# Performance work log

Measured on AMD Instinct MI355X. Metric: run time of the kernel, lower is better.

Reference implementation:

```python
import jax, jax.numpy as jnp
import numpy as np

CS = 64          # chunk_size
CP = CS - 1      # causal_padding
H = 8            # heads
DH = 64          # dim_head
SCALE = DH ** -0.5


def rotate_half(x):
    x1, x2 = jnp.split(x, 2, axis=-1)
    return jnp.concatenate((-x2, x1), axis=-1)


def apply_rope(t, freqs):
    rd = freqs.shape[-1]
    t_rot, t_pass = t[..., :rd], t[..., rd:]
    t_rot = t_rot * jnp.cos(freqs) + rotate_half(t_rot) * jnp.sin(freqs)
    return jnp.concatenate((t_rot, t_pass), axis=-1)


def setup_inputs() -> dict:
    key = jax.random.key(0)
    ks = jax.random.split(key, 10)
    b, n, dim = 4, 4096, 1024
    k_chunks, r, rlen = 64, 2, 128
    inner = H * DH
    return {
        "x": jax.random.normal(ks[0], (b, n, dim), dtype=jnp.float32),
        "context": jax.random.normal(ks[1], (b, k_chunks, r, rlen, dim), dtype=jnp.float32),
        "q_pos_emb": jax.random.normal(ks[2], (1, 1, CS, DH), dtype=jnp.float32),
        "k_pos_emb": jax.random.normal(ks[3], (1, 1, rlen, DH), dtype=jnp.float32),
        "Wq": jax.random.normal(ks[4], (dim, inner), dtype=jnp.float32) * 0.02,
        "Wk": jax.random.normal(ks[5], (dim, inner), dtype=jnp.float32) * 0.02,
        "Wv": jax.random.normal(ks[6], (dim, inner), dtype=jnp.float32) * 0.02,
        "Wo": jax.random.normal(ks[7], (inner, dim), dtype=jnp.float32) * 0.02,
        "bo": jnp.zeros((dim,), dtype=jnp.float32),
        "null_k": jax.random.normal(ks[8], (inner,), dtype=jnp.float32),
        "null_v": jax.random.normal(ks[9], (inner,), dtype=jnp.float32),
    }


def reference(x, context, q_pos_emb, k_pos_emb, Wq, Wk, Wv, Wo, bo, null_k, null_v):
    b, n, dim = x.shape
    _, k_chunks, r, rlen, _ = context.shape
    # causal shift: drop first CP tokens, pad CP zeros at end (F.pad with -CP)
    xs = jnp.pad(x[:, CP:], ((0, 0), (0, CP), (0, 0)))
    seq_index = (n // CS) * CS
    rem = n - seq_index
    xs = xs[:, :seq_index]                                   # [b, k*CS, dim]
    # shift q rope the same way; pad region gets freqs=0 -> identity rotation
    qpe = jnp.pad(q_pos_emb[:, :, CP:], ((0, 0), (0, 0), (0, CP), (0, 0)))
    kpe = jnp.tile(k_pos_emb, (1, 1, r, 1))                  # [1,1,r*rlen,DH]
    bk = b * k_chunks
    xc = xs.reshape(bk, CS, dim)
    ctx = context.reshape(bk, r * rlen, dim)
    # projections -> [bk, h, seq, dh]
    q = (xc @ Wq).reshape(bk, CS, H, DH).transpose(0, 2, 1, 3) * SCALE
    k = (ctx @ Wk).reshape(bk, r * rlen, H, DH).transpose(0, 2, 1, 3)
    v = (ctx @ Wv).reshape(bk, r * rlen, H, DH).transpose(0, 2, 1, 3)
    q = apply_rope(q, qpe)
    k = apply_rope(k, kpe)
    # null kv prepend
    nk = jnp.broadcast_to(null_k.reshape(1, H, 1, DH), (bk, H, 1, DH))
    nv = jnp.broadcast_to(null_v.reshape(1, H, 1, DH), (bk, H, 1, DH))
    k = jnp.concatenate((nk, k), axis=2)
    v = jnp.concatenate((nv, v), axis=2)
    sim = jnp.einsum('bhid,bhjd->bhij', q, k)
    attn = jax.nn.softmax(sim, axis=-1)
    o = jnp.einsum('bhij,bhjd->bhid', attn, v)
    o = o.transpose(0, 2, 1, 3).reshape(bk, CS, H * DH)
    o = o @ Wo + bo                                          # [bk, CS, dim]
    o = o.reshape(b, k_chunks * CS, dim)
    # unshift: pad CP zeros at front, trim CP - rem from end
    o = jnp.concatenate(
        (jnp.zeros((b, CP, dim), o.dtype), o[:, :k_chunks * CS - CP + rem]), axis=1)
    return o
```

## Files before the change

kernel.cpp:

```cpp
#include <hip/hip_runtime.h>


#define DEV __device__ __forceinline__

typedef __bf16 bf16x8 __attribute__((ext_vector_type(8)));
typedef float f32x4 __attribute__((ext_vector_type(4)));

DEV unsigned short f2bf(float f) {
  union { float f; unsigned int u; } v; v.f = f;
  unsigned int u = v.u;
  unsigned int r = (u + 0x7FFFu + ((u >> 16) & 1u)) >> 16;
  return (unsigned short)r;
}
DEV float bf2f(unsigned short h) {
  union { unsigned int u; float f; } v; v.u = ((unsigned int)h) << 16;
  return v.f;
}

DEV void ldst16(const void* g, void* l) {
  __builtin_amdgcn_global_load_lds(
      (const __attribute__((address_space(1))) void*)g,
      (__attribute__((address_space(3))) void*)l, 16, 0, 0);
}

__global__ __launch_bounds__(256) void prep_k(const float* __restrict__ Wq,
                                              const float* __restrict__ Wk,
                                              const float* __restrict__ Wv,
                                              const float* __restrict__ Wo,
                                              const float* __restrict__ qpe,
                                              const float* __restrict__ kpe,
                                              unsigned short* __restrict__ Wqt,
                                              unsigned short* __restrict__ Wkt,
                                              unsigned short* __restrict__ Wvt,
                                              unsigned short* __restrict__ Wot,
                                              float* __restrict__ ck, float* __restrict__ sk,
                                              float* __restrict__ cq, float* __restrict__ sq,
                                              float* __restrict__ out) {
  int blk = blockIdx.x;
  if (blk < 8192) {
    int idx = blk * 256 + threadIdx.x;
    int which = idx >> 19;
    int loc = idx & 524287;
    if (which < 3) {
      int k = loc & 1023, n = loc >> 10;
      const float* W = which == 0 ? Wq : (which == 1 ? Wk : Wv);
      unsigned short* Wt = which == 0 ? Wqt : (which == 1 ? Wkt : Wvt);
      float scale = which == 0 ? 0.125f : 1.0f;
      Wt[loc] = f2bf(W[(size_t)k * 512 + n] * scale);
    } else {
      int k = loc & 511, n = loc >> 9;
      Wot[loc] = f2bf(Wo[(size_t)k * 1024 + n]);
    }
  } else if (blk < 8444) {
    int r = blk - 8192;
    int b = r / 63, rr = r % 63;
    float4 z = {0.f, 0.f, 0.f, 0.f};
    *(float4*)(out + (((size_t)(b * 4096 + rr)) << 10) + threadIdx.x * 4) = z;
  } else {
    int t = (blk - 8444) * 256 + threadIdx.x;
    float f = kpe[t];
    ck[t] = cosf(f);
    sk[t] = sinf(f);
    if (t < 64) {
      float g = qpe[63 * 64 + t];
      cq[t] = cosf(g);
      sq[t] = sinf(g);
    }
  }
}

__global__ __launch_bounds__(256) void cast_k(const float* __restrict__ ctx,
                                              const float* __restrict__ x,
                                              unsigned short* __restrict__ ctxb,
                                              unsigned short* __restrict__ xq) {
  int blk = blockIdx.x;
  if (blk < 32768) {
    size_t i = ((size_t)blk * 256 + threadIdx.x) * 8;
    float4 a = *(const float4*)(ctx + i);
    float4 b = *(const float4*)(ctx + i + 4);
    union { uint4 v; unsigned short s[8]; } u;
    u.s[0] = f2bf(a.x); u.s[1] = f2bf(a.y); u.s[2] = f2bf(a.z); u.s[3] = f2bf(a.w);
    u.s[4] = f2bf(b.x); u.s[5] = f2bf(b.y); u.s[6] = f2bf(b.z); u.s[7] = f2bf(b.w);
    *(uint4*)(ctxb + i) = u.v;
  } else {
    size_t flat = ((size_t)(blk - 32768) * 256 + threadIdx.x) * 8;
    int row = (int)(flat >> 10);
    int c = (int)(flat & 1023);
    int b = row >> 12, p = row & 4095;
    union { uint4 v; unsigned short s[8]; } u;
    if (p <= 4032) {
      const float* sp = x + (((size_t)(b << 12) + p + 63) << 10) + c;
      float4 a = *(const float4*)sp;
      float4 d = *(const float4*)(sp + 4);
      u.s[0] = f2bf(a.x); u.s[1] = f2bf(a.y); u.s[2] = f2bf(a.z); u.s[3] = f2bf(a.w);
      u.s[4] = f2bf(d.x); u.s[5] = f2bf(d.y); u.s[6] = f2bf(d.z); u.s[7] = f2bf(d.w);
    } else {
      #pragma unroll
      for (int e = 0; e < 8; ++e) u.s[e] = 0;
    }
    *(uint4*)(xq + flat) = u.v;
  }
}

template <int MODE>
__global__ __launch_bounds__(256) void gemm_proj(const unsigned short* __restrict__ A,
                                                 const unsigned short* __restrict__ B0,
                                                 const unsigned short* __restrict__ B1,
                                                 unsigned short* __restrict__ out0,
                                                 unsigned short* __restrict__ out1,
                                                 const float* __restrict__ ck,
                                                 const float* __restrict__ sk,
                                                 const float* __restrict__ cq,
                                                 const float* __restrict__ sq,
                                                 int M, int K) {
  __shared__ unsigned short sh[16384];
  unsigned short* As = sh;
  unsigned short* Bs = sh + 8192;

  int id = blockIdx.x;
  int x, y, z;
  if (MODE == 0) { y = id & 3; x = id >> 2; z = 0; }
  else           { y = id & 3; z = (id >> 2) & 1; x = id >> 3; }
  const unsigned short* B = z ? B1 : B0;
  int m0 = x * 128, n0 = y * 128;
  int tid = threadIdx.x, w = tid >> 6, lane = tid & 63;
  int wm = (w & 1) * 64, wn = (w >> 1) * 64;
  int Lrow = lane >> 3, Lc = lane & 7;
  int srcC = Lc ^ (Lrow & 7);

  f32x4 acc[4][4] = {};

  for (int k0 = 0; k0 < K; k0 += 64) {
    #pragma unroll
    for (int q = 0; q < 4; ++q) {
      int t = w * 4 + q;
      ldst16(A + (size_t)(m0 + t * 8 + Lrow) * K + (k0 + srcC * 8), (char*)As + t * 1024);
      ldst16(B + (size_t)(n0 + t * 8 + Lrow) * K + (k0 + srcC * 8), (char*)Bs + t * 1024);
    }
    __syncthreads();
    #pragma unroll
    for (int k32 = 0; k32 < 2; ++k32) {
      int c = k32 * 4 + (lane >> 4);
      bf16x8 af[4], bfr[4];
      #pragma unroll
      for (int mt = 0; mt < 4; ++mt) {
        int m = wm + mt * 16 + (lane & 15);
        af[mt] = *(const bf16x8*)((const char*)As + m * 128 + (c ^ (m & 7)) * 16);
      }
      #pragma unroll
      for (int nt = 0; nt < 4; ++nt) {
        int n = wn + nt * 16 + (lane & 15);
        bfr[nt] = *(const bf16x8*)((const char*)Bs + n * 128 + (c ^ (n & 7)) * 16);
      }
      #pragma unroll
      for (int mt = 0; mt < 4; ++mt)
        #pragma unroll
        for (int nt = 0; nt < 4; ++nt)
          acc[mt][nt] = __builtin_amdgcn_mfma_f32_16x16x32_bf16(af[mt], bfr[nt], acc[mt][nt], 0, 0, 0);
    }
    __syncthreads();
  }

  if (MODE == 0) {
    #pragma unroll
    for (int mt = 0; mt < 4; ++mt)
      #pragma unroll
      for (int nt = 0; nt < 4; ++nt)
        #pragma unroll
        for (int r = 0; r < 4; ++r) {
          int m = m0 + wm + mt * 16 + (lane >> 4) * 4 + r;
          int n = n0 + wn + nt * 16 + (lane & 15);
          float val = acc[mt][nt][r];
          if ((m & 63) == 0) {
            int d = nt * 16 + (lane & 15);
            float partner = acc[mt][nt ^ 2][r];
            val = val * cq[d] + (nt < 2 ? -partner : partner) * sq[d];
          }
          out0[(size_t)m * 512 + n] = f2bf(val);
        }
  } else if (z == 0) {
    #pragma unroll
    for (int mt = 0; mt < 4; ++mt)
      #pragma unroll
      for (int r = 0; r < 4; ++r) {
        int m = m0 + wm + mt * 16 + (lane >> 4) * 4 + r;
        int fib = (m & 127) * 64;
        #pragma unroll
        for (int nt = 0; nt < 4; ++nt) {
          int n = n0 + wn + nt * 16 + (lane & 15);
          int d = nt * 16 + (lane & 15);
          float partner = acc[mt][nt ^ 2][r];
          float val = acc[mt][nt][r] * ck[fib + d] + (nt < 2 ? -partner : partner) * sk[fib + d];
          out0[(size_t)m * 512 + n] = f2bf(val);
        }
      }
  } else {
    #pragma unroll
    for (int mt = 0; mt < 4; ++mt)
      #pragma unroll
      for (int nt = 0; nt < 4; ++nt)
        #pragma unroll
        for (int r = 0; r < 4; ++r) {
          int ml = wm + mt * 16 + (lane >> 4) * 4 + r;
          int nl = wn + nt * 16 + (lane & 15);
          int mc = ml >> 3, me = ml & 7;
          *(unsigned short*)((char*)sh + nl * 256 + ((mc ^ (nl & 15)) * 16) + me * 2) =
              f2bf(acc[mt][nt][r]);
        }
    __syncthreads();
    #pragma unroll
    for (int i = 0; i < 8; ++i) {
      int flat = i * 256 + tid;
      int nl = flat >> 4, mc = flat & 15;
      uint4 v = *(const uint4*)((const char*)sh + nl * 256 + ((mc ^ (nl & 15)) * 16));
      *(uint4*)(out1 + (size_t)(n0 + nl) * M + m0 + mc * 8) = v;
    }
  }
}

__global__ __launch_bounds__(256) void gemm_out(const unsigned short* __restrict__ A,
                                                const unsigned short* __restrict__ B,
                                                const float* __restrict__ bias,
                                                float* __restrict__ out) {
  __shared__ unsigned short sh[16384];
  unsigned short* As = sh;
  unsigned short* Bs = sh + 8192;
  const int K = 512, N = 1024;
  int id = blockIdx.x;
  int y = id & 7, x = id >> 3;
  int m0 = x * 128, n0 = y * 128;
  int tid = threadIdx.x, w = tid >> 6, lane = tid & 63;
  int wm = (w & 1) * 64, wn = (w >> 1) * 64;
  int Lrow = lane >> 3, Lc = lane & 7;
  int srcC = Lc ^ (Lrow & 7);

  f32x4 acc[4][4] = {};

  for (int k0 = 0; k0 < K; k0 += 64) {
    #pragma unroll
    for (int q = 0; q < 4; ++q) {
      int t = w * 4 + q;
      ldst16(A + (size_t)(m0 + t * 8 + Lrow) * K + (k0 + srcC * 8), (char*)As + t * 1024);
      ldst16(B + (size_t)(n0 + t * 8 + Lrow) * K + (k0 + srcC * 8), (char*)Bs + t * 1024);
    }
    __syncthreads();
    #pragma unroll
    for (int k32 = 0; k32 < 2; ++k32) {
      int c = k32 * 4 + (lane >> 4);
      bf16x8 af[4], bfr[4];
      #pragma unroll
      for (int mt = 0; mt < 4; ++mt) {
        int m = wm + mt * 16 + (lane & 15);
        af[mt] = *(const bf16x8*)((const char*)As + m * 128 + (c ^ (m & 7)) * 16);
      }
      #pragma unroll
      for (int nt = 0; nt < 4; ++nt) {
        int n = wn + nt * 16 + (lane & 15);
        bfr[nt] = *(const bf16x8*)((const char*)Bs + n * 128 + (c ^ (n & 7)) * 16);
      }
      #pragma unroll
      for (int mt = 0; mt < 4; ++mt)
        #pragma unroll
        for (int nt = 0; nt < 4; ++nt)
          acc[mt][nt] = __builtin_amdgcn_mfma_f32_16x16x32_bf16(af[mt], bfr[nt], acc[mt][nt], 0, 0, 0);
    }
    __syncthreads();
  }
  #pragma unroll
  for (int mt = 0; mt < 4; ++mt)
    #pragma unroll
    for (int nt = 0; nt < 4; ++nt)
      #pragma unroll
      for (int r = 0; r < 4; ++r) {
        int m = m0 + wm + mt * 16 + (lane >> 4) * 4 + r;
        int n = n0 + wn + nt * 16 + (lane & 15);
        int b = m >> 12, t = m & 4095;
        if (t <= 4032)
          out[((size_t)((b << 12) + t + 63)) * N + n] = acc[mt][nt][r] + bias[n];
      }
}

__global__ __launch_bounds__(256) void attn_kernel(const unsigned short* __restrict__ qb,
                                                   const unsigned short* __restrict__ kb,
                                                   const unsigned short* __restrict__ vtg,
                                                   const float* __restrict__ nullk,
                                                   const float* __restrict__ nullv,
                                                   unsigned short* __restrict__ ob) {
  __shared__ unsigned short qs[64 * 64];
  __shared__ unsigned short ks[256 * 64];
  __shared__ unsigned short ps[64 * 256];
  __shared__ float rnull[64];
  __shared__ float rsum[64];
  int id = blockIdx.x;
  int bc = (id & 7) + 8 * (id >> 6);
  int h = (id >> 3) & 7;
  int tid = threadIdx.x, w = tid >> 6, lane = tid & 63;
  int Lrow = lane >> 3, Lc = lane & 7, srcC = Lc ^ (Lrow & 7);

  #pragma unroll
  for (int q8 = 0; q8 < 2; ++q8) {
    int t = w * 2 + q8;
    ldst16(qb + (size_t)(bc * 64 + t * 8 + Lrow) * 512 + h * 64 + srcC * 8, (char*)qs + t * 1024);
  }
  #pragma unroll
  for (int q8 = 0; q8 < 8; ++q8) {
    int t = w * 8 + q8;
    ldst16(kb + (size_t)(bc * 256 + t * 8 + Lrow) * 512 + h * 64 + srcC * 8, (char*)ks + t * 1024);
  }
  __syncthreads();

  {
    int rl = lane >> 2, part = lane & 3;
    int row = w * 16 + rl;
    float s = 0.f;
    #pragma unroll
    for (int e = 0; e < 16; ++e) {
      int d = part * 16 + e;
      unsigned short qv = *(const unsigned short*)((const char*)qs + row * 128 +
                                                   (((d >> 3) ^ (row & 7)) * 16) + (d & 7) * 2);
      s += bf2f(qv) * nullk[h * 64 + d];
    }
    s += __shfl_xor(s, 1);
    s += __shfl_xor(s, 2);
    if (part == 0) rnull[row] = s;
  }

  f32x4 acc[16] = {};
  #pragma unroll
  for (int k32 = 0; k32 < 2; ++k32) {
    int c = k32 * 4 + (lane >> 4);
    int m = w * 16 + (lane & 15);
    bf16x8 a = *(const bf16x8*)((const char*)qs + m * 128 + (c ^ (m & 7)) * 16);
    #pragma unroll
    for (int nt = 0; nt < 16; ++nt) {
      int n = nt * 16 + (lane & 15);
      bf16x8 b = *(const bf16x8*)((const char*)ks + n * 128 + (c ^ (n & 7)) * 16);
      acc[nt] = __builtin_amdgcn_mfma_f32_16x16x32_bf16(a, b, acc[nt], 0, 0, 0);
    }
  }

  int g = lane >> 4;
  #pragma unroll
  for (int r = 0; r < 4; ++r) {
    int row = w * 16 + g * 4 + r;
    float mx = -3.0e38f;
    #pragma unroll
    for (int nt = 0; nt < 16; ++nt) mx = fmaxf(mx, acc[nt][r]);
    mx = fmaxf(mx, __shfl_xor(mx, 1));
    mx = fmaxf(mx, __shfl_xor(mx, 2));
    mx = fmaxf(mx, __shfl_xor(mx, 4));
    mx = fmaxf(mx, __shfl_xor(mx, 8));
    float ns = rnull[row];
    float mm = fmaxf(mx, ns);
    float s = 0.f;
    #pragma unroll
    for (int nt = 0; nt < 16; ++nt) {
      float p = __expf(acc[nt][r] - mm);
      acc[nt][r] = p;
      s += p;
    }
    s += __shfl_xor(s, 1);
    s += __shfl_xor(s, 2);
    s += __shfl_xor(s, 4);
    s += __shfl_xor(s, 8);
    float en = __expf(ns - mm);
    s += en;
    if ((lane & 15) == 0) {
      rsum[row] = s;
      rnull[row] = en;
    }
  }

  #pragma unroll
  for (int nt = 0; nt < 16; ++nt)
    #pragma unroll
    for (int r = 0; r < 4; ++r) {
      int row = w * 16 + g * 4 + r;
      int col = nt * 16 + (lane & 15);
      *(unsigned short*)((char*)ps + row * 512 + (((col >> 3) ^ (row & 7)) * 16) + (col & 7) * 2) =
          f2bf(acc[nt][r]);
    }
  __syncthreads();

  #pragma unroll
  for (int q8 = 0; q8 < 8; ++q8) {
    int t = w * 8 + q8;
    int dd = t * 2 + (lane >> 5);
    int cl = (lane & 31) ^ (dd & 7);
    ldst16(vtg + (size_t)(h * 64 + dd) * 65536 + bc * 256 + cl * 8, (char*)ks + t * 1024);
  }
  __syncthreads();

  f32x4 oacc[4] = {};
  #pragma unroll
  for (int k32 = 0; k32 < 8; ++k32) {
    int c = k32 * 4 + (lane >> 4);
    int m = w * 16 + (lane & 15);
    bf16x8 a = *(const bf16x8*)((const char*)ps + m * 512 + (c ^ (m & 7)) * 16);
    #pragma unroll
    for (int nt = 0; nt < 4; ++nt) {
      int n = nt * 16 + (lane & 15);
      bf16x8 b = *(const bf16x8*)((const char*)ks + n * 512 + (c ^ (n & 7)) * 16);
      oacc[nt] = __builtin_amdgcn_mfma_f32_16x16x32_bf16(a, b, oacc[nt], 0, 0, 0);
    }
  }
  #pragma unroll
  for (int nt = 0; nt < 4; ++nt)
    #pragma unroll
    for (int r = 0; r < 4; ++r) {
      int row = w * 16 + g * 4 + r;
      int d = nt * 16 + (lane & 15);
      float o = oacc[nt][r] + rnull[row] * nullv[h * 64 + d];
      o /= rsum[row];
      ob[((size_t)(bc * 64 + row) * 8 + h) * 64 + d] = f2bf(o);
    }
}

extern "C" void kernel_launch(void* const* d_in, const int* in_sizes, int n_in,
                              void* d_out, int out_size, void* d_ws, size_t ws_size,
                              hipStream_t stream) {
  const float* x = (const float*)d_in[0];
  const float* ctx = (const float*)d_in[1];
  const float* qpe = (const float*)d_in[2];
  const float* kpe = (const float*)d_in[3];
  const float* Wq = (const float*)d_in[4];
  const float* Wk = (const float*)d_in[5];
  const float* Wv = (const float*)d_in[6];
  const float* Wo = (const float*)d_in[7];
  const float* bo = (const float*)d_in[8];
  const float* nk = (const float*)d_in[9];
  const float* nv = (const float*)d_in[10];
  float* out = (float*)d_out;
  char* ws = (char*)d_ws;

  unsigned short* xq   = (unsigned short*)(ws + 0);
  unsigned short* ctxb = (unsigned short*)(ws + 33554432);
  unsigned short* Wqt  = (unsigned short*)(ws + 167772160);
  unsigned short* Wkt  = (unsigned short*)(ws + 168820736);
  unsigned short* Wvt  = (unsigned short*)(ws + 169869312);
  unsigned short* Wot  = (unsigned short*)(ws + 170917888);
  unsigned short* qb   = (unsigned short*)(ws + 171966464);
  unsigned short* kb   = (unsigned short*)(ws + 188743680);
  unsigned short* vtg  = (unsigned short*)(ws + 255852544);
  unsigned short* obuf = (unsigned short*)(ws + 322961408);
  float* cosk = (float*)(ws + 339738624);
  float* sink = (float*)(ws + 339771392);
  float* cosq = (float*)(ws + 339804160);
  float* sinq = (float*)(ws + 339804416);

  prep_k<<<8476, 256, 0, stream>>>(Wq, Wk, Wv, Wo, qpe, kpe, Wqt, Wkt, Wvt, Wot,
                                   cosk, sink, cosq, sinq, out);
  cast_k<<<40960, 256, 0, stream>>>(ctx, x, ctxb, xq);

  gemm_proj<0><<<512, 256, 0, stream>>>(xq, Wqt, Wqt, qb, nullptr,
                                        cosk, sink, cosq, sinq, 16384, 1024);
  gemm_proj<1><<<4096, 256, 0, stream>>>(ctxb, Wkt, Wvt, kb, vtg,
                                         cosk, sink, cosq, sinq, 65536, 1024);

  attn_kernel<<<2048, 256, 0, stream>>>(qb, kb, vtg, nk, nv, obuf);

  gemm_out<<<1024, 256, 0, stream>>>(obuf, Wot, bo, out);
}
```

Before: 804.5 us.

## Fuse fp32-to-bf16 casts into projection GEMM loads and drop softmax max

```diff
diff --git a/kernel.cpp b/kernel.cpp
--- a/kernel.cpp
+++ b/kernel.cpp
@@ -15,6 +15,9 @@
 DEV float bf2f(unsigned short h) {
   union { unsigned int u; float f; } v; v.u = ((unsigned int)h) << 16;
   return v.f;
+}
+DEV unsigned int pkbf(unsigned int hi, unsigned int lo) {
+  return __builtin_amdgcn_perm(hi, lo, 0x07060302u);
 }
 
 DEV void ldst16(const void* g, void* l) {
@@ -69,41 +72,8 @@
   }
 }
 
-__global__ __launch_bounds__(256) void cast_k(const float* __restrict__ ctx,
-                                              const float* __restrict__ x,
-                                              unsigned short* __restrict__ ctxb,
-                                              unsigned short* __restrict__ xq) {
-  int blk = blockIdx.x;
-  if (blk < 32768) {
-    size_t i = ((size_t)blk * 256 + threadIdx.x) * 8;
-    float4 a = *(const float4*)(ctx + i);
-    float4 b = *(const float4*)(ctx + i + 4);
-    union { uint4 v; unsigned short s[8]; } u;
-    u.s[0] = f2bf(a.x); u.s[1] = f2bf(a.y); u.s[2] = f2bf(a.z); u.s[3] = f2bf(a.w);
-    u.s[4] = f2bf(b.x); u.s[5] = f2bf(b.y); u.s[6] = f2bf(b.z); u.s[7] = f2bf(b.w);
-    *(uint4*)(ctxb + i) = u.v;
-  } else {
-    size_t flat = ((size_t)(blk - 32768) * 256 + threadIdx.x) * 8;
-    int row = (int)(flat >> 10);
-    int c = (int)(flat & 1023);
-    int b = row >> 12, p = row & 4095;
-    union { uint4 v; unsigned short s[8]; } u;
-    if (p <= 4032) {
-      const float* sp = x + (((size_t)(b << 12) + p + 63) << 10) + c;
-      float4 a = *(const float4*)sp;
-      float4 d = *(const float4*)(sp + 4);
-      u.s[0] = f2bf(a.x); u.s[1] = f2bf(a.y); u.s[2] = f2bf(a.z); u.s[3] = f2bf(a.w);
-      u.s[4] = f2bf(d.x); u.s[5] = f2bf(d.y); u.s[6] = f2bf(d.z); u.s[7] = f2bf(d.w);
-    } else {
-      #pragma unroll
-      for (int e = 0; e < 8; ++e) u.s[e] = 0;
-    }
-    *(uint4*)(xq + flat) = u.v;
-  }
-}
-
 template <int MODE>
-__global__ __launch_bounds__(256) void gemm_proj(const unsigned short* __restrict__ A,
+__global__ __launch_bounds__(256) void gemm_proj(const float* __restrict__ Af,
                                                  const unsigned short* __restrict__ B0,
                                                  const unsigned short* __restrict__ B1,
                                                  unsigned short* __restrict__ out0,
@@ -111,16 +81,16 @@
                                                  const float* __restrict__ ck,
                                                  const float* __restrict__ sk,
                                                  const float* __restrict__ cq,
-                                                 const float* __restrict__ sq,
-                                                 int M, int K) {
+                                                 const float* __restrict__ sq) {
   __shared__ unsigned short sh[16384];
   unsigned short* As = sh;
   unsigned short* Bs = sh + 8192;
+  const int K = 1024;
 
   int id = blockIdx.x;
   int x, y, z;
-  if (MODE == 0) { y = id & 3; x = id >> 2; z = 0; }
-  else           { y = id & 3; z = (id >> 2) & 1; x = id >> 3; }
+  if (MODE == 0) { x = (id & 7) + 8 * (id >> 5); y = (id >> 3) & 3; z = 0; }
+  else           { x = (id & 7) + 8 * (id >> 6); int j = (id >> 3) & 7; y = j & 3; z = j >> 2; }
   const unsigned short* B = z ? B1 : B0;
   int m0 = x * 128, n0 = y * 128;
   int tid = threadIdx.x, w = tid >> 6, lane = tid & 63;
@@ -128,13 +98,39 @@
   int Lrow = lane >> 3, Lc = lane & 7;
   int srcC = Lc ^ (Lrow & 7);
 
+  const float* asrc[4];
+  bool avalid[4];
+  #pragma unroll
+  for (int q = 0; q < 4; ++q) {
+    int t = w * 4 + q;
+    int gm = m0 + t * 8 + Lrow;
+    if (MODE == 0) {
+      int b = gm >> 12, p = gm & 4095;
+      avalid[q] = (p <= 4032);
+      asrc[q] = Af + (((size_t)(b << 12) + p + 63) << 10) + srcC * 8;
+    } else {
+      avalid[q] = true;
+      asrc[q] = Af + (size_t)gm * 1024 + srcC * 8;
+    }
+  }
+
   f32x4 acc[4][4] = {};
 
   for (int k0 = 0; k0 < K; k0 += 64) {
     #pragma unroll
     for (int q = 0; q < 4; ++q) {
       int t = w * 4 + q;
-      ldst16(A + (size_t)(m0 + t * 8 + Lrow) * K + (k0 + srcC * 8), (char*)As + t * 1024);
+      uint4 lo = {0, 0, 0, 0}, hi = {0, 0, 0, 0};
+      if (avalid[q]) {
+        lo = *(const uint4*)(asrc[q] + k0);
+        hi = *(const uint4*)(asrc[q] + k0 + 4);
+      }
+      uint4 pk;
+      pk.x = pkbf(lo.y, lo.x);
+      pk.y = pkbf(lo.w, lo.z);
+      pk.z = pkbf(hi.y, hi.x);
+      pk.w = pkbf(hi.w, hi.z);
+      *(uint4*)((char*)As + t * 1024 + lane * 16) = pk;
       ldst16(B + (size_t)(n0 + t * 8 + Lrow) * K + (k0 + srcC * 8), (char*)Bs + t * 1024);
     }
     __syncthreads();
@@ -213,7 +209,7 @@
       int flat = i * 256 + tid;
       int nl = flat >> 4, mc = flat & 15;
       uint4 v = *(const uint4*)((const char*)sh + nl * 256 + ((mc ^ (nl & 15)) * 16));
-      *(uint4*)(out1 + (size_t)(n0 + nl) * M + m0 + mc * 8) = v;
+      *(uint4*)(out1 + (size_t)(n0 + nl) * 65536 + m0 + mc * 8) = v;
     }
   }
 }
@@ -227,7 +223,7 @@
   unsigned short* Bs = sh + 8192;
   const int K = 512, N = 1024;
   int id = blockIdx.x;
-  int y = id & 7, x = id >> 3;
+  int x = (id & 7) + 8 * (id >> 6), y = (id >> 3) & 7;
   int m0 = x * 128, n0 = y * 128;
   int tid = threadIdx.x, w = tid >> 6, lane = tid & 63;
   int wm = (w & 1) * 64, wn = (w >> 1) * 64;
@@ -322,7 +318,7 @@
     }
     s += __shfl_xor(s, 1);
     s += __shfl_xor(s, 2);
-    if (part == 0) rnull[row] = s;
+    if (part == 0) rnull[row] = __expf(s);
   }
 
   f32x4 acc[16] = {};
@@ -343,19 +339,10 @@
   #pragma unroll
   for (int r = 0; r < 4; ++r) {
     int row = w * 16 + g * 4 + r;
-    float mx = -3.0e38f;
-    #pragma unroll
-    for (int nt = 0; nt < 16; ++nt) mx = fmaxf(mx, acc[nt][r]);
-    mx = fmaxf(mx, __shfl_xor(mx, 1));
-    mx = fmaxf(mx, __shfl_xor(mx, 2));
-    mx = fmaxf(mx, __shfl_xor(mx, 4));
-    mx = fmaxf(mx, __shfl_xor(mx, 8));
-    float ns = rnull[row];
-    float mm = fmaxf(mx, ns);
     float s = 0.f;
     #pragma unroll
     for (int nt = 0; nt < 16; ++nt) {
-      float p = __expf(acc[nt][r] - mm);
+      float p = __expf(acc[nt][r]);
       acc[nt][r] = p;
       s += p;
     }
@@ -363,12 +350,7 @@
     s += __shfl_xor(s, 2);
     s += __shfl_xor(s, 4);
     s += __shfl_xor(s, 8);
-    float en = __expf(ns - mm);
-    s += en;
-    if ((lane & 15) == 0) {
-      rsum[row] = s;
-      rnull[row] = en;
-    }
+    if ((lane & 15) == 0) rsum[row] = s + rnull[row];
   }
 
   #pragma unroll
@@ -433,29 +415,26 @@
   float* out = (float*)d_out;
   char* ws = (char*)d_ws;
 
-  unsigned short* xq   = (unsigned short*)(ws + 0);
-  unsigned short* ctxb = (unsigned short*)(ws + 33554432);
-  unsigned short* Wqt  = (unsigned short*)(ws + 167772160);
-  unsigned short* Wkt  = (unsigned short*)(ws + 168820736);
-  unsigned short* Wvt  = (unsigned short*)(ws + 169869312);
-  unsigned short* Wot  = (unsigned short*)(ws + 170917888);
-  unsigned short* qb   = (unsigned short*)(ws + 171966464);
-  unsigned short* kb   = (unsigned short*)(ws + 188743680);
-  unsigned short* vtg  = (unsigned short*)(ws + 255852544);
-  unsigned short* obuf = (unsigned short*)(ws + 322961408);
-  float* cosk = (float*)(ws + 339738624);
-  float* sink = (float*)(ws + 339771392);
-  float* cosq = (float*)(ws + 339804160);
-  float* sinq = (float*)(ws + 339804416);
+  unsigned short* Wqt  = (unsigned short*)(ws + 0);
+  unsigned short* Wkt  = (unsigned short*)(ws + 1048576);
+  unsigned short* Wvt  = (unsigned short*)(ws + 2097152);
+  unsigned short* Wot  = (unsigned short*)(ws + 3145728);
+  unsigned short* qb   = (unsigned short*)(ws + 4194304);
+  unsigned short* kb   = (unsigned short*)(ws + 20971520);
+  unsigned short* vtg  = (unsigned short*)(ws + 88080384);
+  unsigned short* obuf = (unsigned short*)(ws + 155189248);
+  float* cosk = (float*)(ws + 171966464);
+  float* sink = (float*)(ws + 171999232);
+  float* cosq = (float*)(ws + 172032000);
+  float* sinq = (float*)(ws + 172032256);
 
   prep_k<<<8476, 256, 0, stream>>>(Wq, Wk, Wv, Wo, qpe, kpe, Wqt, Wkt, Wvt, Wot,
                                    cosk, sink, cosq, sinq, out);
-  cast_k<<<40960, 256, 0, stream>>>(ctx, x, ctxb, xq);
-
-  gemm_proj<0><<<512, 256, 0, stream>>>(xq, Wqt, Wqt, qb, nullptr,
-                                        cosk, sink, cosq, sinq, 16384, 1024);
-  gemm_proj<1><<<4096, 256, 0, stream>>>(ctxb, Wkt, Wvt, kb, vtg,
-                                         cosk, sink, cosq, sinq, 65536, 1024);
+
+  gemm_proj<0><<<512, 256, 0, stream>>>(x, Wqt, Wqt, qb, nullptr,
+                                        cosk, sink, cosq, sinq);
+  gemm_proj<1><<<4096, 256, 0, stream>>>(ctx, Wkt, Wvt, kb, vtg,
+                                         cosk, sink, cosq, sinq);
 
   attn_kernel<<<2048, 256, 0, stream>>>(qb, kb, vtg, nk, nv, obuf);
 
```

Measured after the change: 764.6 us. -5.0%, faster.
